# Optimization experiments

Hardware: AMD Instinct MI355X
Metric: run time of the kernel (lower is better)

The kernel has to match this reference:

```python
import jax, jax.numpy as jnp
import numpy as np

B, F, D_IN, D_K, D_V = 4, 4096, 1024, 128, 128


def setup_inputs() -> dict:
    key = jax.random.key(0)
    ks = jax.random.split(key, 7)
    s_in = 1.0 / np.sqrt(D_IN)
    x = jax.random.normal(ks[0], (B, F, D_IN), dtype=jnp.float32)
    # nn.Linear weights stored as (out, in); we keep (in, out) for x @ W
    Wq = jax.random.uniform(ks[1], (D_IN, D_K), jnp.float32, -s_in, s_in)
    bq = jax.random.uniform(ks[2], (D_K,), jnp.float32, -s_in, s_in)
    Wk = jax.random.uniform(ks[3], (D_IN, D_K), jnp.float32, -s_in, s_in)
    bk = jax.random.uniform(ks[4], (D_K,), jnp.float32, -s_in, s_in)
    Wv = jax.random.uniform(ks[5], (D_IN, D_V), jnp.float32, -s_in, s_in)
    bv = jax.random.uniform(ks[6], (D_V,), jnp.float32, -s_in, s_in)
    return {"x": x, "Wq": Wq, "bq": bq, "Wk": Wk, "bk": bk, "Wv": Wv, "bv": bv}


def reference(x, Wq, bq, Wk, bk, Wv, bv):
    Q = x @ Wq + bq  # (B, F, d_k)
    K = x @ Wk + bk  # (B, F, d_k)
    V = x @ Wv + bv  # (B, F, d_v)
    scale = 1.0 / jnp.sqrt(jnp.asarray(Q.shape[-1], Q.dtype))
    scores = jnp.einsum('bqd,bkd->bqk', Q, K) * scale  # (B, F, F)
    attn = jax.nn.softmax(scores, axis=-1)
    return jnp.einsum('bqk,bkd->bqd', attn, V)  # (B, F, d_v)
```

## Files before the change

### kernel.cpp

```cpp
#include <hip/hip_runtime.h>

#define TB 4
#define TF 4096
#define DIN 1024
#define DK 128
#define M_TOT (TB * TF)

typedef __attribute__((ext_vector_type(8))) short sh8;
typedef __attribute__((ext_vector_type(4))) float f32x4;

#if __has_builtin(__builtin_amdgcn_exp2f)
#define EXP2(x) __builtin_amdgcn_exp2f(x)
#else
#define EXP2(x) exp2f(x)
#endif

__device__ __forceinline__ unsigned short f2bf(float f) {
  unsigned int u = __builtin_bit_cast(unsigned int, f);
  u += 0x7FFFu + ((u >> 16) & 1u);
  return (unsigned short)(u >> 16);
}

__device__ __forceinline__ unsigned int pack_bf2(float a, float b) {
  return (unsigned int)f2bf(a) | ((unsigned int)f2bf(b) << 16);
}

__device__ __forceinline__ float bf2f(unsigned short u) {
  unsigned int x = ((unsigned int)u) << 16;
  return __builtin_bit_cast(float, x);
}

__global__ __launch_bounds__(256) void prep_wt_kernel(
    const float* __restrict__ Wq, const float* __restrict__ Wk,
    const float* __restrict__ Wv, unsigned short* __restrict__ Wf) {
  int idx = blockIdx.x * 256 + threadIdx.x;
  int j = idx & 7;
  int lane = (idx >> 3) & 63;
  int ks = (idx >> 9) & 31;
  int t = (idx >> 14) & 7;
  int p = idx >> 17;
  int col = t * 16 + (lane & 15);
  int k = ks * 32 + (lane >> 4) * 8 + j;
  const float* W = (p == 0) ? Wq : (p == 1) ? Wk : Wv;
  Wf[idx] = f2bf(W[k * DK + col]);
}

__global__ __launch_bounds__(512, 2) void proj_kernel(
    const float* __restrict__ x,
    const unsigned short* __restrict__ Wf,
    const float* __restrict__ bq, const float* __restrict__ bk,
    const float* __restrict__ bv,
    unsigned short* __restrict__ Qb,
    unsigned short* __restrict__ Kb,
    unsigned short* __restrict__ VT)
{
  const int tid = threadIdx.x;
  const int wave = tid >> 6;
  const int lane = tid & 63;
  const int lr = lane & 15;
  const int lg = lane >> 4;
  const int m0 = blockIdx.x * 64;
  const int col = wave * 16 + lr;

  __shared__ unsigned short Xlds[64 * 32];

  f32x4 acc[3][4];
  const f32x4 z4 = {0.f, 0.f, 0.f, 0.f};
#pragma unroll
  for (int p = 0; p < 3; ++p)
#pragma unroll
    for (int m = 0; m < 4; ++m) acc[p][m] = z4;

  const int xr = tid >> 3;
  const int xk = (tid & 7) * 4;

  for (int k0 = 0; k0 < DIN; k0 += 32) {
    const float4 f = *(const float4*)(x + (size_t)(m0 + xr) * DIN + k0 + xk);
    ushort4 w4;
    w4.x = f2bf(f.x); w4.y = f2bf(f.y); w4.z = f2bf(f.z); w4.w = f2bf(f.w);
    __syncthreads();
    *(ushort4*)&Xlds[xr * 32 + xk] = w4;
    __syncthreads();

    sh8 a[4];
#pragma unroll
    for (int m = 0; m < 4; ++m)
      a[m] = *(const sh8*)&Xlds[(m * 16 + lr) * 32 + lg * 8];
#pragma unroll
    for (int p = 0; p < 3; ++p) {
      sh8 b = *(const sh8*)(Wf + ((size_t)((p * 8 + wave) * 32 + (k0 >> 5))) *
                                     512 + lane * 8);
#pragma unroll
      for (int m = 0; m < 4; ++m)
        acc[p][m] =
            __builtin_amdgcn_mfma_f32_16x16x32_bf16(a[m], b, acc[p][m], 0, 0, 0);
    }
  }

  const float scale = 0.12751744f;
  const int b_idx = m0 >> 12;
  const float add_q = bq[col];
  const float add_k = bk[col];
  const float add_v = bv[col];
#pragma unroll
  for (int m = 0; m < 4; ++m) {
    const int rowbase = m0 + m * 16 + lg * 4;
#pragma unroll
    for (int r = 0; r < 4; ++r) {
      Qb[(size_t)(rowbase + r) * DK + col] =
          f2bf((acc[0][m][r] + add_q) * scale);
      Kb[(size_t)(rowbase + r) * DK + col] = f2bf(acc[1][m][r] + add_k);
    }
    const int fbase = (m0 & (TF - 1)) + m * 16 + lg * 4;
    ushort4 pv;
    pv.x = f2bf(acc[2][m][0] + add_v);
    pv.y = f2bf(acc[2][m][1] + add_v);
    pv.z = f2bf(acc[2][m][2] + add_v);
    pv.w = f2bf(acc[2][m][3] + add_v);
    *(ushort4*)(VT + ((size_t)b_idx * DK + col) * TF + fbase) = pv;
  }
}

template <int SPLIT>
__global__ __launch_bounds__(512, 2) void attn_part_kernel(
    const unsigned short* __restrict__ Qb, const unsigned short* __restrict__ Kb,
    const unsigned short* __restrict__ VT, unsigned short* __restrict__ Opart,
    float* __restrict__ Mpart, float* __restrict__ Lpart,
    float* __restrict__ out) {
  constexpr int CHUNK = TF / SPLIT;
  const int tid = threadIdx.x;
  const int lane = tid & 63;
  const int lr = lane & 15;
  const int lg = lane >> 4;

  const int bid = blockIdx.x;
  const int xcd = bid & 7;
  const int batch = xcd >> 1;
  const int idb = ((bid >> 3) << 1) | (xcd & 1);
  const int slot = idb / SPLIT;
  const int chunk = idb % SPLIT;
  const int wave = tid >> 6;
  const int q0 = batch * TF + slot * 128 + wave * 16;
  const int kbase = chunk * CHUNK;

  __shared__ unsigned short Klds[64 * 136];
  __shared__ unsigned short Vlds[128 * 72];

  const unsigned short* Qp = Qb + (size_t)q0 * DK;
  const unsigned short* Kp = Kb + (size_t)batch * TF * DK;
  const unsigned short* Vp = VT + (size_t)batch * DK * TF;

  sh8 aq[4];
#pragma unroll
  for (int dd = 0; dd < 4; ++dd)
    aq[dd] = *(const sh8*)(Qp + lr * DK + dd * 32 + lg * 8);

  const f32x4 z4 = {0.f, 0.f, 0.f, 0.f};
  f32x4 ot[8];
#pragma unroll
  for (int nb = 0; nb < 8; ++nb) ot[nb] = z4;
  float mrow = -1e30f, lrow = 0.f;

  const int srcA = lr + ((lane >> 4) & 1) * 32;
  const int srcB = srcA + 16;
  const bool chi = (lg >= 2);

  for (int kk0 = kbase; kk0 < kbase + CHUNK; kk0 += 64) {
    __syncthreads();
#pragma unroll
    for (int i = 0; i < 2; ++i) {
      int c = tid + i * 512;
      int row = c >> 4, c8 = c & 15;
      *(uint4*)&Klds[row * 136 + c8 * 8] =
          *(const uint4*)(Kp + (size_t)(kk0 + row) * DK + c8 * 8);
    }
#pragma unroll
    for (int i = 0; i < 2; ++i) {
      int c = tid + i * 512;
      int row = c >> 3, c8 = c & 7;
      *(uint4*)&Vlds[row * 72 + c8 * 8] =
          *(const uint4*)(Vp + (size_t)row * TF + kk0 + c8 * 8);
    }
    __syncthreads();

    f32x4 st[4];
#pragma unroll
    for (int c = 0; c < 4; ++c) st[c] = z4;
#pragma unroll
    for (int dd = 0; dd < 4; ++dd) {
#pragma unroll
      for (int c = 0; c < 4; ++c) {
        sh8 kb = *(const sh8*)&Klds[(c * 16 + lr) * 136 + dd * 32 + lg * 8];
        st[c] =
            __builtin_amdgcn_mfma_f32_16x16x32_bf16(kb, aq[dd], st[c], 0, 0, 0);
      }
    }

    float mx = st[0][0];
#pragma unroll
    for (int c = 0; c < 4; ++c)
#pragma unroll
      for (int r = 0; r < 4; ++r) mx = fmaxf(mx, st[c][r]);
    mx = fmaxf(mx, __shfl_xor(mx, 16));
    mx = fmaxf(mx, __shfl_xor(mx, 32));

    if (!__all(mx - mrow <= 11.5f)) {
      const float mnew = fmaxf(mrow, mx);
      const float al = EXP2(mrow - mnew);
      lrow *= al;
#pragma unroll
      for (int nb = 0; nb < 8; ++nb)
#pragma unroll
        for (int r = 0; r < 4; ++r) ot[nb][r] *= al;
      mrow = mnew;
    }

    float p[4][4];
    float rs = 0.f;
#pragma unroll
    for (int c = 0; c < 4; ++c)
#pragma unroll
      for (int r = 0; r < 4; ++r) {
        p[c][r] = EXP2(st[c][r] - mrow);
        rs += p[c][r];
      }
    rs += __shfl_xor(rs, 16);
    rs += __shfl_xor(rs, 32);
    lrow += rs;

    unsigned int up[4][2];
#pragma unroll
    for (int c = 0; c < 4; ++c) {
      up[c][0] = pack_bf2(p[c][0], p[c][1]);
      up[c][1] = pack_bf2(p[c][2], p[c][3]);
    }

#pragma unroll
    for (int ks = 0; ks < 2; ++ks) {
      unsigned int e0 = __shfl((int)up[2 * ks][0], srcA);
      unsigned int o0 = __shfl((int)up[2 * ks + 1][0], srcA);
      unsigned int e1 = __shfl((int)up[2 * ks][1], srcA);
      unsigned int o1 = __shfl((int)up[2 * ks + 1][1], srcA);
      unsigned int e2 = __shfl((int)up[2 * ks][0], srcB);
      unsigned int o2 = __shfl((int)up[2 * ks + 1][0], srcB);
      unsigned int e3 = __shfl((int)up[2 * ks][1], srcB);
      unsigned int o3 = __shfl((int)up[2 * ks + 1][1], srcB);
      union { unsigned int u[4]; sh8 v; } PA;
      PA.u[0] = chi ? o0 : e0;
      PA.u[1] = chi ? o1 : e1;
      PA.u[2] = chi ? o2 : e2;
      PA.u[3] = chi ? o3 : e3;
#pragma unroll
      for (int nb = 0; nb < 8; ++nb) {
        sh8 vb = *(const sh8*)&Vlds[(nb * 16 + lr) * 72 + ks * 32 + lg * 8];
        ot[nb] =
            __builtin_amdgcn_mfma_f32_16x16x32_bf16(vb, PA.v, ot[nb], 0, 0, 0);
      }
    }
  }

  if constexpr (SPLIT == 1) {
    const float inv = 1.0f / lrow;
#pragma unroll
    for (int nb = 0; nb < 8; ++nb) {
      float4 res = {ot[nb][0] * inv, ot[nb][1] * inv, ot[nb][2] * inv,
                    ot[nb][3] * inv};
      *(float4*)(out + (size_t)(q0 + lr) * DK + nb * 16 + lg * 4) = res;
    }
  } else {
    const int row = q0 + lr;
    if (lg == 0) {
      Mpart[(size_t)chunk * M_TOT + row] = mrow;
      Lpart[(size_t)chunk * M_TOT + row] = lrow;
    }
#pragma unroll
    for (int nb = 0; nb < 8; ++nb) {
      ushort4 res;
      res.x = f2bf(ot[nb][0]); res.y = f2bf(ot[nb][1]);
      res.z = f2bf(ot[nb][2]); res.w = f2bf(ot[nb][3]);
      *(ushort4*)(Opart + ((size_t)chunk * M_TOT + row) * DK + nb * 16 +
                  lg * 4) = res;
    }
  }
}

__global__ __launch_bounds__(256) void combine_kernel(
    const unsigned short* __restrict__ Opart, const float* __restrict__ Mpart,
    const float* __restrict__ Lpart, float* __restrict__ out, int split) {
  const int idx = blockIdx.x * 256 + threadIdx.x;
  const int row = idx >> 5;
  const int cq = (idx & 31) << 2;
  float m = -1e30f;
  for (int s = 0; s < split; ++s) m = fmaxf(m, Mpart[(size_t)s * M_TOT + row]);
  float den = 0.f;
  float4 acc = {0.f, 0.f, 0.f, 0.f};
  for (int s = 0; s < split; ++s) {
    const float w = EXP2(Mpart[(size_t)s * M_TOT + row] - m);
    den += w * Lpart[(size_t)s * M_TOT + row];
    const ushort4 v =
        *(const ushort4*)(Opart + ((size_t)s * M_TOT + row) * DK + cq);
    acc.x += w * bf2f(v.x); acc.y += w * bf2f(v.y);
    acc.z += w * bf2f(v.z); acc.w += w * bf2f(v.w);
  }
  const float inv = 1.0f / den;
  float4 res = {acc.x * inv, acc.y * inv, acc.z * inv, acc.w * inv};
  *(float4*)(out + (size_t)row * DK + cq) = res;
}

extern "C" void kernel_launch(void* const* d_in, const int* in_sizes, int n_in,
                              void* d_out, int out_size, void* d_ws,
                              size_t ws_size, hipStream_t stream) {
  const float* x = (const float*)d_in[0];
  const float* Wq = (const float*)d_in[1];
  const float* bq = (const float*)d_in[2];
  const float* Wk = (const float*)d_in[3];
  const float* bk = (const float*)d_in[4];
  const float* Wv = (const float*)d_in[5];
  const float* bv = (const float*)d_in[6];
  float* out = (float*)d_out;

  unsigned short* Wf = (unsigned short*)d_ws;
  unsigned short* Qb = Wf + 3 * DK * DIN;
  unsigned short* Kb = Qb + (size_t)M_TOT * DK;
  unsigned short* VT = Kb + (size_t)M_TOT * DK;
  unsigned short* Opart = VT + (size_t)M_TOT * DK;
  const size_t base_bytes = 2ull * (3 * DK * DIN + 3ull * M_TOT * DK);
  const size_t per_split = (size_t)M_TOT * DK * 2 + 2ull * M_TOT * 4;

  prep_wt_kernel<<<(3 * DK * DIN) / 256, 256, 0, stream>>>(Wq, Wk, Wv, Wf);
  proj_kernel<<<M_TOT / 64, 512, 0, stream>>>(x, Wf, bq, bk, bv, Qb, Kb, VT);

  int split;
  if (ws_size >= base_bytes + 4 * per_split) split = 4;
  else if (ws_size >= base_bytes + 2 * per_split) split = 2;
  else split = 1;

  float* Mpart = (float*)(Opart + (size_t)split * M_TOT * DK);
  float* Lpart = Mpart + (size_t)split * M_TOT;

  if (split == 4) {
    attn_part_kernel<4><<<128 * 4, 512, 0, stream>>>(Qb, Kb, VT, Opart, Mpart,
                                                     Lpart, out);
    combine_kernel<<<M_TOT * 32 / 256, 256, 0, stream>>>(Opart, Mpart, Lpart,
                                                         out, 4);
  } else if (split == 2) {
    attn_part_kernel<2><<<128 * 2, 512, 0, stream>>>(Qb, Kb, VT, Opart, Mpart,
                                                     Lpart, out);
    combine_kernel<<<M_TOT * 32 / 256, 256, 0, stream>>>(Opart, Mpart, Lpart,
                                                         out, 2);
  } else {
    attn_part_kernel<1><<<128, 512, 0, stream>>>(Qb, Kb, VT, nullptr, nullptr,
                                                 nullptr, out);
  }
}
```

Before: 109.3 us.

## Process two 16-row query groups per wave and raise KV split to 8

Each wave now handles 32 query rows (two 16-row groups) instead of 16, so every K and V fragment read from LDS feeds two MFMAs. A block covers 256 queries, which halves the K/V LDS loads per query. To keep enough blocks in flight, the launcher adds a split-8 path along the key dimension when workspace allows. The change doubles the accumulator and Q register footprint per wave, which may cut occupancy or cause spills under launch_bounds(512,2), and the extra split makes the combine pass read more partial results.

```diff
diff --git a/kernel.cpp b/kernel.cpp
--- a/kernel.cpp
+++ b/kernel.cpp
@@ -140,7 +140,7 @@
   const int slot = idb / SPLIT;
   const int chunk = idb % SPLIT;
   const int wave = tid >> 6;
-  const int q0 = batch * TF + slot * 128 + wave * 16;
+  const int q0 = batch * TF + slot * 256 + wave * 32;
   const int kbase = chunk * CHUNK;
 
   __shared__ unsigned short Klds[64 * 136];
@@ -150,16 +150,21 @@
   const unsigned short* Kp = Kb + (size_t)batch * TF * DK;
   const unsigned short* Vp = VT + (size_t)batch * DK * TF;
 
-  sh8 aq[4];
-#pragma unroll
-  for (int dd = 0; dd < 4; ++dd)
-    aq[dd] = *(const sh8*)(Qp + lr * DK + dd * 32 + lg * 8);
+  sh8 aq[2][4];
+#pragma unroll
+  for (int g = 0; g < 2; ++g)
+#pragma unroll
+    for (int dd = 0; dd < 4; ++dd)
+      aq[g][dd] =
+          *(const sh8*)(Qp + (g * 16 + lr) * DK + dd * 32 + lg * 8);
 
   const f32x4 z4 = {0.f, 0.f, 0.f, 0.f};
-  f32x4 ot[8];
-#pragma unroll
-  for (int nb = 0; nb < 8; ++nb) ot[nb] = z4;
-  float mrow = -1e30f, lrow = 0.f;
+  f32x4 ot[2][8];
+#pragma unroll
+  for (int g = 0; g < 2; ++g)
+#pragma unroll
+    for (int nb = 0; nb < 8; ++nb) ot[g][nb] = z4;
+  float mrow[2] = {-1e30f, -1e30f}, lrow[2] = {0.f, 0.f};
 
   const int srcA = lr + ((lane >> 4) & 1) * 32;
   const int srcB = srcA + 16;
@@ -183,103 +188,118 @@
     }
     __syncthreads();
 
-    f32x4 st[4];
-#pragma unroll
-    for (int c = 0; c < 4; ++c) st[c] = z4;
+    f32x4 st[2][4];
+#pragma unroll
+    for (int g = 0; g < 2; ++g)
+#pragma unroll
+      for (int c = 0; c < 4; ++c) st[g][c] = z4;
 #pragma unroll
     for (int dd = 0; dd < 4; ++dd) {
 #pragma unroll
       for (int c = 0; c < 4; ++c) {
         sh8 kb = *(const sh8*)&Klds[(c * 16 + lr) * 136 + dd * 32 + lg * 8];
-        st[c] =
-            __builtin_amdgcn_mfma_f32_16x16x32_bf16(kb, aq[dd], st[c], 0, 0, 0);
-      }
-    }
-
-    float mx = st[0][0];
-#pragma unroll
-    for (int c = 0; c < 4; ++c)
-#pragma unroll
-      for (int r = 0; r < 4; ++r) mx = fmaxf(mx, st[c][r]);
-    mx = fmaxf(mx, __shfl_xor(mx, 16));
-    mx = fmaxf(mx, __shfl_xor(mx, 32));
-
-    if (!__all(mx - mrow <= 11.5f)) {
-      const float mnew = fmaxf(mrow, mx);
-      const float al = EXP2(mrow - mnew);
-      lrow *= al;
-#pragma unroll
-      for (int nb = 0; nb < 8; ++nb)
-#pragma unroll
-        for (int r = 0; r < 4; ++r) ot[nb][r] *= al;
-      mrow = mnew;
-    }
-
-    float p[4][4];
-    float rs = 0.f;
-#pragma unroll
-    for (int c = 0; c < 4; ++c)
-#pragma unroll
-      for (int r = 0; r < 4; ++r) {
-        p[c][r] = EXP2(st[c][r] - mrow);
-        rs += p[c][r];
-      }
-    rs += __shfl_xor(rs, 16);
-    rs += __shfl_xor(rs, 32);
-    lrow += rs;
-
-    unsigned int up[4][2];
-#pragma unroll
-    for (int c = 0; c < 4; ++c) {
-      up[c][0] = pack_bf2(p[c][0], p[c][1]);
-      up[c][1] = pack_bf2(p[c][2], p[c][3]);
+        st[0][c] = __builtin_amdgcn_mfma_f32_16x16x32_bf16(kb, aq[0][dd],
+                                                           st[0][c], 0, 0, 0);
+        st[1][c] = __builtin_amdgcn_mfma_f32_16x16x32_bf16(kb, aq[1][dd],
+                                                           st[1][c], 0, 0, 0);
+      }
+    }
+
+    unsigned int up[2][4][2];
+#pragma unroll
+    for (int g = 0; g < 2; ++g) {
+      float mx = st[g][0][0];
+#pragma unroll
+      for (int c = 0; c < 4; ++c)
+#pragma unroll
+        for (int r = 0; r < 4; ++r) mx = fmaxf(mx, st[g][c][r]);
+      mx = fmaxf(mx, __shfl_xor(mx, 16));
+      mx = fmaxf(mx, __shfl_xor(mx, 32));
+
+      if (!__all(mx - mrow[g] <= 11.5f)) {
+        const float mnew = fmaxf(mrow[g], mx);
+        const float al = EXP2(mrow[g] - mnew);
+        lrow[g] *= al;
+#pragma unroll
+        for (int nb = 0; nb < 8; ++nb)
+#pragma unroll
+          for (int r = 0; r < 4; ++r) ot[g][nb][r] *= al;
+        mrow[g] = mnew;
+      }
+
+      float rs = 0.f;
+#pragma unroll
+      for (int c = 0; c < 4; ++c) {
+        float p0 = EXP2(st[g][c][0] - mrow[g]);
+        float p1 = EXP2(st[g][c][1] - mrow[g]);
+        float p2 = EXP2(st[g][c][2] - mrow[g]);
+        float p3 = EXP2(st[g][c][3] - mrow[g]);
+        rs += p0 + p1 + p2 + p3;
+        up[g][c][0] = pack_bf2(p0, p1);
+        up[g][c][1] = pack_bf2(p2, p3);
+      }
+      rs += __shfl_xor(rs, 16);
+      rs += __shfl_xor(rs, 32);
+      lrow[g] += rs;
     }
 
 #pragma unroll
     for (int ks = 0; ks < 2; ++ks) {
-      unsigned int e0 = __shfl((int)up[2 * ks][0], srcA);
-      unsigned int o0 = __shfl((int)up[2 * ks + 1][0], srcA);
-      unsigned int e1 = __shfl((int)up[2 * ks][1], srcA);
-      unsigned int o1 = __shfl((int)up[2 * ks + 1][1], srcA);
-      unsigned int e2 = __shfl((int)up[2 * ks][0], srcB);
-      unsigned int o2 = __shfl((int)up[2 * ks + 1][0], srcB);
-      unsigned int e3 = __shfl((int)up[2 * ks][1], srcB);
-      unsigned int o3 = __shfl((int)up[2 * ks + 1][1], srcB);
-      union { unsigned int u[4]; sh8 v; } PA;
-      PA.u[0] = chi ? o0 : e0;
-      PA.u[1] = chi ? o1 : e1;
-      PA.u[2] = chi ? o2 : e2;
-      PA.u[3] = chi ? o3 : e3;
+      union { unsigned int u[4]; sh8 v; } PA[2];
+#pragma unroll
+      for (int g = 0; g < 2; ++g) {
+        unsigned int e0 = __shfl((int)up[g][2 * ks][0], srcA);
+        unsigned int o0 = __shfl((int)up[g][2 * ks + 1][0], srcA);
+        unsigned int e1 = __shfl((int)up[g][2 * ks][1], srcA);
+        unsigned int o1 = __shfl((int)up[g][2 * ks + 1][1], srcA);
+        unsigned int e2 = __shfl((int)up[g][2 * ks][0], srcB);
+        unsigned int o2 = __shfl((int)up[g][2 * ks + 1][0], srcB);
+        unsigned int e3 = __shfl((int)up[g][2 * ks][1], srcB);
+        unsigned int o3 = __shfl((int)up[g][2 * ks + 1][1], srcB);
+        PA[g].u[0] = chi ? o0 : e0;
+        PA[g].u[1] = chi ? o1 : e1;
+        PA[g].u[2] = chi ? o2 : e2;
+        PA[g].u[3] = chi ? o3 : e3;
+      }
 #pragma unroll
       for (int nb = 0; nb < 8; ++nb) {
         sh8 vb = *(const sh8*)&Vlds[(nb * 16 + lr) * 72 + ks * 32 + lg * 8];
-        ot[nb] =
-            __builtin_amdgcn_mfma_f32_16x16x32_bf16(vb, PA.v, ot[nb], 0, 0, 0);
+        ot[0][nb] = __builtin_amdgcn_mfma_f32_16x16x32_bf16(vb, PA[0].v,
+                                                            ot[0][nb], 0, 0, 0);
+        ot[1][nb] = __builtin_amdgcn_mfma_f32_16x16x32_bf16(vb, PA[1].v,
+                                                            ot[1][nb], 0, 0, 0);
       }
     }
   }
 
   if constexpr (SPLIT == 1) {
-    const float inv = 1.0f / lrow;
-#pragma unroll
-    for (int nb = 0; nb < 8; ++nb) {
-      float4 res = {ot[nb][0] * inv, ot[nb][1] * inv, ot[nb][2] * inv,
-                    ot[nb][3] * inv};
-      *(float4*)(out + (size_t)(q0 + lr) * DK + nb * 16 + lg * 4) = res;
+#pragma unroll
+    for (int g = 0; g < 2; ++g) {
+      const float inv = 1.0f / lrow[g];
+#pragma unroll
+      for (int nb = 0; nb < 8; ++nb) {
+        float4 res = {ot[g][nb][0] * inv, ot[g][nb][1] * inv,
+                      ot[g][nb][2] * inv, ot[g][nb][3] * inv};
+        *(float4*)(out + (size_t)(q0 + g * 16 + lr) * DK + nb * 16 + lg * 4) =
+            res;
+      }
     }
   } else {
-    const int row = q0 + lr;
-    if (lg == 0) {
-      Mpart[(size_t)chunk * M_TOT + row] = mrow;
-      Lpart[(size_t)chunk * M_TOT + row] = lrow;
-    }
-#pragma unroll
-    for (int nb = 0; nb < 8; ++nb) {
-      ushort4 res;
-      res.x = f2bf(ot[nb][0]); res.y = f2bf(ot[nb][1]);
-      res.z = f2bf(ot[nb][2]); res.w = f2bf(ot[nb][3]);
-      *(ushort4*)(Opart + ((size_t)chunk * M_TOT + row) * DK + nb * 16 +
-                  lg * 4) = res;
+#pragma unroll
+    for (int g = 0; g < 2; ++g) {
+      const int row = q0 + g * 16 + lr;
+      if (lg == 0) {
+        Mpart[(size_t)chunk * M_TOT + row] = mrow[g];
+        Lpart[(size_t)chunk * M_TOT + row] = lrow[g];
+      }
+#pragma unroll
+      for (int nb = 0; nb < 8; ++nb) {
+        ushort4 res;
+        res.x = f2bf(ot[g][nb][0]); res.y = f2bf(ot[g][nb][1]);
+        res.z = f2bf(ot[g][nb][2]); res.w = f2bf(ot[g][nb][3]);
+        *(ushort4*)(Opart + ((size_t)chunk * M_TOT + row) * DK + nb * 16 +
+                    lg * 4) = res;
+      }
     }
   }
 }
@@ -331,25 +351,31 @@
   proj_kernel<<<M_TOT / 64, 512, 0, stream>>>(x, Wf, bq, bk, bv, Qb, Kb, VT);
 
   int split;
-  if (ws_size >= base_bytes + 4 * per_split) split = 4;
+  if (ws_size >= base_bytes + 8 * per_split) split = 8;
+  else if (ws_size >= base_bytes + 4 * per_split) split = 4;
   else if (ws_size >= base_bytes + 2 * per_split) split = 2;
   else split = 1;
 
   float* Mpart = (float*)(Opart + (size_t)split * M_TOT * DK);
   float* Lpart = Mpart + (size_t)split * M_TOT;
 
-  if (split == 4) {
-    attn_part_kernel<4><<<128 * 4, 512, 0, stream>>>(Qb, Kb, VT, Opart, Mpart,
-                                                     Lpart, out);
+  if (split == 8) {
+    attn_part_kernel<8><<<64 * 8, 512, 0, stream>>>(Qb, Kb, VT, Opart, Mpart,
+                                                    Lpart, out);
+    combine_kernel<<<M_TOT * 32 / 256, 256, 0, stream>>>(Opart, Mpart, Lpart,
+                                                         out, 8);
+  } else if (split == 4) {
+    attn_part_kernel<4><<<64 * 4, 512, 0, stream>>>(Qb, Kb, VT, Opart, Mpart,
+                                                    Lpart, out);
     combine_kernel<<<M_TOT * 32 / 256, 256, 0, stream>>>(Opart, Mpart, Lpart,
                                                          out, 4);
   } else if (split == 2) {
-    attn_part_kernel<2><<<128 * 2, 512, 0, stream>>>(Qb, Kb, VT, Opart, Mpart,
-                                                     Lpart, out);
+    attn_part_kernel<2><<<64 * 2, 512, 0, stream>>>(Qb, Kb, VT, Opart, Mpart,
+                                                    Lpart, out);
     combine_kernel<<<M_TOT * 32 / 256, 256, 0, stream>>>(Opart, Mpart, Lpart,
                                                          out, 2);
   } else {
-    attn_part_kernel<1><<<128, 512, 0, stream>>>(Qb, Kb, VT, nullptr, nullptr,
-                                                 nullptr, out);
-  }
-}
+    attn_part_kernel<1><<<64, 512, 0, stream>>>(Qb, Kb, VT, nullptr, nullptr,
+                                                nullptr, out);
+  }
+}
```

New measurement: 123.6 us. 1.13x slower.
